# Kernel tuning notes

Hardware: AMD Instinct MI355X
Metric: run time of the kernel (lower is better)

Reference implementation:

```python
import jax, jax.numpy as jnp
import numpy as np

TOP_K = 8
NUM_EXPERTS = 128
HIDDEN = 2048
TOKENS = 16384
NORM_TOPK_PROB = True


def setup_inputs() -> dict:
    key = jax.random.key(0)
    k1, k2 = jax.random.split(key)
    hidden_states = jax.random.normal(k1, (TOKENS, HIDDEN), dtype=jnp.float32)
    # gate weight [num_experts, hidden] (nn.Linear layout)
    weight = jax.random.normal(k2, (NUM_EXPERTS, HIDDEN), dtype=jnp.float32) * 0.02
    return {"hidden_states": hidden_states, "weight": weight}


def reference(hidden_states, weight):
    x = hidden_states.reshape(-1, HIDDEN)
    # router_logits: [tokens, num_experts]
    router_logits = jnp.einsum("td,ed->te", x, weight)
    router_probs = jax.nn.softmax(router_logits.astype(jnp.float32), axis=-1)
    top_vals, top_idx = jax.lax.top_k(router_probs, TOP_K)
    if NORM_TOPK_PROB:
        top_vals = top_vals / jnp.sum(top_vals, axis=-1, keepdims=True)
    top_vals = top_vals.astype(hidden_states.dtype)
    return router_logits, top_vals, top_idx
```

## Files before the change

### kernel.cpp

```cpp
#include <hip/hip_runtime.h>
#include <float.h>
#include <math.h>

#define TOKENS 16384
#define HIDDEN 2048
#define NEXP 128
#define TOPK 8
#define NCAND 12
#define DELTA 5e-4f

#define BM 32
#define BK 64
#define KITERS (HIDDEN / BK)

typedef float f32x16 __attribute__((ext_vector_type(16)));
typedef short bf16x8 __attribute__((ext_vector_type(8)));

__device__ __forceinline__ unsigned pack_hi(float a, float b) {
    return (__float_as_uint(a) >> 16) | (__float_as_uint(b) & 0xFFFF0000u);
}
__device__ __forceinline__ float resid(float a) {
    return a - __uint_as_float(__float_as_uint(a) & 0xFFFF0000u);
}

__device__ __forceinline__ void load_lds_16B(const void* g, void* l) {
    __builtin_amdgcn_global_load_lds(
        (const __attribute__((address_space(1))) unsigned int*)g,
        (__attribute__((address_space(3))) unsigned int*)l, 16, 0, 0);
}

__global__ __launch_bounds__(256) void presplit_w(const float* __restrict__ W,
                                                  unsigned short* __restrict__ Ws) {
    const int c = blockIdx.x * 256 + threadIdx.x;
    const int lane = c & 63;
    const int q = c >> 6;
    const int hl = q & 1;
    const int nt = (q >> 1) & 3;
    const int k16 = q >> 3;
    const int e = nt * 32 + (lane & 31);
    const int k0 = k16 * 16 + (lane >> 5) * 8;
    const float* wp = W + (size_t)e * HIDDEN + k0;
    float4 a = *(const float4*)wp;
    float4 b = *(const float4*)(wp + 4);
    if (hl) {
        a.x = resid(a.x); a.y = resid(a.y); a.z = resid(a.z); a.w = resid(a.w);
        b.x = resid(b.x); b.y = resid(b.y); b.z = resid(b.z); b.w = resid(b.w);
    }
    uint4 o;
    o.x = pack_hi(a.x, a.y); o.y = pack_hi(a.z, a.w);
    o.z = pack_hi(b.x, b.y); o.w = pack_hi(b.z, b.w);
    *(uint4*)(Ws + (size_t)c * 8) = o;
}

__global__ __launch_bounds__(256) void router_gemm(const float* __restrict__ X,
                                                   const unsigned short* __restrict__ Ws,
                                                   float* __restrict__ logits) {
    __shared__ unsigned short sA[8 * 512];
    __shared__ unsigned short sB[32 * 512];
    const int tid = threadIdx.x;
    const int lane = tid & 63;
    const int wid = tid >> 6;
    const int t0 = blockIdx.x * BM;

    const int arow = tid >> 3, aq = tid & 7;
    const int offH = ((aq >> 1) * 2 + 0) * 512 + ((aq & 1) * 32 + arow) * 8;
    const int offL = offH + 512;
    const float* Xp = X + (size_t)(t0 + arow) * HIDDEN + aq * 8;

    f32x16 acc;
#pragma unroll
    for (int r = 0; r < 16; ++r) acc[r] = 0.f;

    float4 xa = *(const float4*)(Xp);
    float4 xb = *(const float4*)(Xp + 4);

#pragma unroll 1
    for (int kt = 0; kt < KITERS; ++kt) {
        __syncthreads();
        {
            const unsigned short* src = Ws + ((size_t)kt * 32 + wid * 8) * 512 + lane * 8;
            unsigned short* dst = &sB[(wid * 8) * 512];
#pragma unroll
            for (int i = 0; i < 8; ++i)
                load_lds_16B(src + i * 512, dst + i * 512);
        }
        {
            uint4 v;
            v.x = pack_hi(xa.x, xa.y); v.y = pack_hi(xa.z, xa.w);
            v.z = pack_hi(xb.x, xb.y); v.w = pack_hi(xb.z, xb.w);
            *(uint4*)&sA[offH] = v;
            v.x = pack_hi(resid(xa.x), resid(xa.y));
            v.y = pack_hi(resid(xa.z), resid(xa.w));
            v.z = pack_hi(resid(xb.x), resid(xb.y));
            v.w = pack_hi(resid(xb.z), resid(xb.w));
            *(uint4*)&sA[offL] = v;
        }
        __syncthreads();

        if (kt + 1 < KITERS) {
            const float* xp = Xp + (kt + 1) * BK;
            xa = *(const float4*)(xp);
            xb = *(const float4*)(xp + 4);
        }

#pragma unroll
        for (int s = 0; s < 4; ++s) {
            const bf16x8 ah = *(const bf16x8*)&sA[(s * 2 + 0) * 512 + lane * 8];
            const bf16x8 al = *(const bf16x8*)&sA[(s * 2 + 1) * 512 + lane * 8];
            const int bb = (s * 8 + wid * 2) * 512 + lane * 8;
            const bf16x8 bh = *(const bf16x8*)&sB[bb];
            const bf16x8 bl = *(const bf16x8*)&sB[bb + 512];
            acc = __builtin_amdgcn_mfma_f32_32x32x16_bf16(ah, bh, acc, 0, 0, 0);
            acc = __builtin_amdgcn_mfma_f32_32x32x16_bf16(ah, bl, acc, 0, 0, 0);
            acc = __builtin_amdgcn_mfma_f32_32x32x16_bf16(al, bh, acc, 0, 0, 0);
        }
    }

    const int e = wid * 32 + (lane & 31);
    const int rbase = 4 * (lane >> 5);
#pragma unroll
    for (int reg = 0; reg < 16; ++reg) {
        const int row = (reg & 3) + 8 * (reg >> 2) + rbase;
        logits[(size_t)(t0 + row) * NEXP + e] = acc[reg];
    }
}

__global__ __launch_bounds__(256) void router_topk(const float* __restrict__ logits,
                                                   const float* __restrict__ X,
                                                   const float* __restrict__ W,
                                                   float* __restrict__ top_vals,
                                                   float* __restrict__ top_idx) {
    const int lane = threadIdx.x & 63;
    const int t = blockIdx.x * 4 + (threadIdx.x >> 6);
    const float* lrow = logits + (size_t)t * NEXP;
    const float l0 = lrow[lane];
    const float l1 = lrow[lane + 64];
    bool r0 = false, r1 = false;
    float vals[NCAND]; int idxs[NCAND];

#pragma unroll
    for (int it = 0; it < TOPK + 1; ++it) {
        const float c0 = r0 ? -FLT_MAX : l0;
        const float c1 = r1 ? -FLT_MAX : l1;
        float v; int id;
        if (c1 > c0) { v = c1; id = lane + 64; }
        else         { v = c0; id = lane; }
#pragma unroll
        for (int off = 1; off < 64; off <<= 1) {
            const float ov = __shfl_xor(v, off);
            const int   oi = __shfl_xor(id, off);
            if (ov > v || (ov == v && oi < id)) { v = ov; id = oi; }
        }
        vals[it] = v; idxs[it] = id;
        if (id == lane) r0 = true;
        else if (id == lane + 64) r1 = true;
    }

    float ming = FLT_MAX;
#pragma unroll
    for (int i = 0; i < TOPK; ++i) ming = fminf(ming, vals[i] - vals[i + 1]);

    if (ming >= DELTA) {
        if (lane == 0) {
            const float m = vals[0];
            float ex[TOPK], s = 0.f;
#pragma unroll
            for (int i = 0; i < TOPK; ++i) { ex[i] = expf(vals[i] - m); s += ex[i]; }
            const float inv = 1.f / s;
#pragma unroll
            for (int i = 0; i < TOPK; ++i) {
                top_vals[(size_t)t * TOPK + i] = ex[i] * inv;
                top_idx[(size_t)t * TOPK + i] = (float)idxs[i];
            }
        }
        return;
    }

#pragma unroll
    for (int it = TOPK + 1; it < NCAND; ++it) {
        const float c0 = r0 ? -FLT_MAX : l0;
        const float c1 = r1 ? -FLT_MAX : l1;
        float v; int id;
        if (c1 > c0) { v = c1; id = lane + 64; }
        else         { v = c0; id = lane; }
#pragma unroll
        for (int off = 1; off < 64; off <<= 1) {
            const float ov = __shfl_xor(v, off);
            const int   oi = __shfl_xor(id, off);
            if (ov > v || (ov == v && oi < id)) { v = ov; id = oi; }
        }
        vals[it] = v; idxs[it] = id;
        if (id == lane) r0 = true;
        else if (id == lane + 64) r1 = true;
    }

    const float* xr = X + (size_t)t * HIDDEN;
    double xd[32];
#pragma unroll
    for (int j = 0; j < 8; ++j) {
        const float4 v = *(const float4*)(xr + j * 256 + lane * 4);
        xd[j * 4 + 0] = (double)v.x; xd[j * 4 + 1] = (double)v.y;
        xd[j * 4 + 2] = (double)v.z; xd[j * 4 + 3] = (double)v.w;
    }
    double acc[NCAND];
#pragma unroll
    for (int c = 0; c < NCAND; ++c) {
        const float* wr = W + (size_t)idxs[c] * HIDDEN;
        double a0 = 0.0, a1 = 0.0;
#pragma unroll
        for (int j = 0; j < 8; ++j) {
            const float4 w = *(const float4*)(wr + j * 256 + lane * 4);
            a0 = fma((double)w.x, xd[j * 4 + 0], a0);
            a1 = fma((double)w.y, xd[j * 4 + 1], a1);
            a0 = fma((double)w.z, xd[j * 4 + 2], a0);
            a1 = fma((double)w.w, xd[j * 4 + 3], a1);
        }
        acc[c] = a0 + a1;
    }
#pragma unroll
    for (int c = 0; c < NCAND; ++c)
#pragma unroll
        for (int off = 1; off < 64; off <<= 1)
            acc[c] += __shfl_xor(acc[c], off);

    int rank[NCAND];
#pragma unroll
    for (int c = 0; c < NCAND; ++c) {
        int r = 0;
#pragma unroll
        for (int m = 0; m < NCAND; ++m)
            if (acc[m] > acc[c] || (acc[m] == acc[c] && idxs[m] < idxs[c])) ++r;
        rank[c] = r;
    }
    double vmax = acc[0];
#pragma unroll
    for (int c = 0; c < NCAND; ++c) if (rank[c] == 0) vmax = acc[c];
    float ex[NCAND], s = 0.f;
#pragma unroll
    for (int c = 0; c < NCAND; ++c) {
        ex[c] = (rank[c] < TOPK) ? expf((float)(acc[c] - vmax)) : 0.f;
        s += ex[c];
    }
    const float inv = 1.f / s;
    if (lane == 0) {
#pragma unroll
        for (int c = 0; c < NCAND; ++c)
            if (rank[c] < TOPK) {
                top_vals[(size_t)t * TOPK + rank[c]] = ex[c] * inv;
                top_idx[(size_t)t * TOPK + rank[c]] = (float)idxs[c];
            }
    }
}

extern "C" void kernel_launch(void* const* d_in, const int* in_sizes, int n_in,
                              void* d_out, int out_size, void* d_ws, size_t ws_size,
                              hipStream_t stream) {
    const float* X = (const float*)d_in[0];
    const float* W = (const float*)d_in[1];
    float* logits = (float*)d_out;
    float* tvals  = logits + (size_t)TOKENS * NEXP;
    float* tidx   = tvals + (size_t)TOKENS * TOPK;

    unsigned short* Wsplit = (unsigned short*)d_ws;

    presplit_w<<<256, 256, 0, stream>>>(W, Wsplit);
    router_gemm<<<TOKENS / BM, 256, 0, stream>>>(X, Wsplit, logits);
    router_topk<<<TOKENS / 4, 256, 0, stream>>>(logits, X, W, tvals, tidx);
}
```

Baseline: 294.9 us.

## Drop LDS staging in router GEMM, load operands directly into registers

The router GEMM no longer stages X and the pre-split W through shared memory. Each wave now loads its own A rows and B fragments straight from global memory into registers, with a 4-deep software prefetch ring and a bare s_barrier per group to keep waves roughly in step. This removes the LDS writes and reads and the two __syncthreads per K tile. In exchange, each of the four waves reloads the same X rows redundantly, which raises global/L2 traffic and register pressure.

```diff
diff --git a/kernel.cpp b/kernel.cpp
--- a/kernel.cpp
+++ b/kernel.cpp
@@ -10,8 +10,7 @@
 #define DELTA 5e-4f
 
 #define BM 32
-#define BK 64
-#define KITERS (HIDDEN / BK)
+#define KSTEPS (HIDDEN / 16)
 
 typedef float f32x16 __attribute__((ext_vector_type(16)));
 typedef short bf16x8 __attribute__((ext_vector_type(8)));
@@ -23,10 +22,17 @@
     return a - __uint_as_float(__float_as_uint(a) & 0xFFFF0000u);
 }
 
-__device__ __forceinline__ void load_lds_16B(const void* g, void* l) {
-    __builtin_amdgcn_global_load_lds(
-        (const __attribute__((address_space(1))) unsigned int*)g,
-        (__attribute__((address_space(3))) unsigned int*)l, 16, 0, 0);
+__device__ __forceinline__ bf16x8 pack8_hi(const float4 a, const float4 b) {
+    union { uint4 u; bf16x8 v; } t;
+    t.u.x = pack_hi(a.x, a.y); t.u.y = pack_hi(a.z, a.w);
+    t.u.z = pack_hi(b.x, b.y); t.u.w = pack_hi(b.z, b.w);
+    return t.v;
+}
+__device__ __forceinline__ bf16x8 pack8_lo(const float4 a, const float4 b) {
+    union { uint4 u; bf16x8 v; } t;
+    t.u.x = pack_hi(resid(a.x), resid(a.y)); t.u.y = pack_hi(resid(a.z), resid(a.w));
+    t.u.z = pack_hi(resid(b.x), resid(b.y)); t.u.w = pack_hi(resid(b.z), resid(b.w));
+    return t.v;
 }
 
 __global__ __launch_bounds__(256) void presplit_w(const float* __restrict__ W,
@@ -55,65 +61,44 @@
 __global__ __launch_bounds__(256) void router_gemm(const float* __restrict__ X,
                                                    const unsigned short* __restrict__ Ws,
                                                    float* __restrict__ logits) {
-    __shared__ unsigned short sA[8 * 512];
-    __shared__ unsigned short sB[32 * 512];
     const int tid = threadIdx.x;
     const int lane = tid & 63;
     const int wid = tid >> 6;
     const int t0 = blockIdx.x * BM;
 
-    const int arow = tid >> 3, aq = tid & 7;
-    const int offH = ((aq >> 1) * 2 + 0) * 512 + ((aq & 1) * 32 + arow) * 8;
-    const int offL = offH + 512;
-    const float* Xp = X + (size_t)(t0 + arow) * HIDDEN + aq * 8;
+    const float* xp = X + (size_t)(t0 + (lane & 31)) * HIDDEN + (lane >> 5) * 8;
+    const unsigned short* bp = Ws + (size_t)(wid * 2) * 512 + (size_t)lane * 8;
 
     f32x16 acc;
 #pragma unroll
     for (int r = 0; r < 16; ++r) acc[r] = 0.f;
 
-    float4 xa = *(const float4*)(Xp);
-    float4 xb = *(const float4*)(Xp + 4);
+    float4 xa[4], xb[4];
+    bf16x8 bh[4], bl[4];
+#pragma unroll
+    for (int i = 0; i < 4; ++i) {
+        xa[i] = *(const float4*)(xp + i * 16);
+        xb[i] = *(const float4*)(xp + i * 16 + 4);
+        bh[i] = *(const bf16x8*)(bp + (size_t)i * 4096);
+        bl[i] = *(const bf16x8*)(bp + (size_t)i * 4096 + 512);
+    }
 
 #pragma unroll 1
-    for (int kt = 0; kt < KITERS; ++kt) {
-        __syncthreads();
-        {
-            const unsigned short* src = Ws + ((size_t)kt * 32 + wid * 8) * 512 + lane * 8;
-            unsigned short* dst = &sB[(wid * 8) * 512];
-#pragma unroll
-            for (int i = 0; i < 8; ++i)
-                load_lds_16B(src + i * 512, dst + i * 512);
-        }
-        {
-            uint4 v;
-            v.x = pack_hi(xa.x, xa.y); v.y = pack_hi(xa.z, xa.w);
-            v.z = pack_hi(xb.x, xb.y); v.w = pack_hi(xb.z, xb.w);
-            *(uint4*)&sA[offH] = v;
-            v.x = pack_hi(resid(xa.x), resid(xa.y));
-            v.y = pack_hi(resid(xa.z), resid(xa.w));
-            v.z = pack_hi(resid(xb.x), resid(xb.y));
-            v.w = pack_hi(resid(xb.z), resid(xb.w));
-            *(uint4*)&sA[offL] = v;
-        }
-        __syncthreads();
-
-        if (kt + 1 < KITERS) {
-            const float* xp = Xp + (kt + 1) * BK;
-            xa = *(const float4*)(xp);
-            xb = *(const float4*)(xp + 4);
-        }
-
-#pragma unroll
-        for (int s = 0; s < 4; ++s) {
-            const bf16x8 ah = *(const bf16x8*)&sA[(s * 2 + 0) * 512 + lane * 8];
-            const bf16x8 al = *(const bf16x8*)&sA[(s * 2 + 1) * 512 + lane * 8];
-            const int bb = (s * 8 + wid * 2) * 512 + lane * 8;
-            const bf16x8 bh = *(const bf16x8*)&sB[bb];
-            const bf16x8 bl = *(const bf16x8*)&sB[bb + 512];
-            acc = __builtin_amdgcn_mfma_f32_32x32x16_bf16(ah, bh, acc, 0, 0, 0);
-            acc = __builtin_amdgcn_mfma_f32_32x32x16_bf16(ah, bl, acc, 0, 0, 0);
-            acc = __builtin_amdgcn_mfma_f32_32x32x16_bf16(al, bh, acc, 0, 0, 0);
-        }
+    for (int kt = 0; kt < KSTEPS; kt += 4) {
+#pragma unroll
+        for (int i = 0; i < 4; ++i) {
+            const bf16x8 ah = pack8_hi(xa[i], xb[i]);
+            const bf16x8 al = pack8_lo(xa[i], xb[i]);
+            acc = __builtin_amdgcn_mfma_f32_32x32x16_bf16(ah, bh[i], acc, 0, 0, 0);
+            acc = __builtin_amdgcn_mfma_f32_32x32x16_bf16(ah, bl[i], acc, 0, 0, 0);
+            acc = __builtin_amdgcn_mfma_f32_32x32x16_bf16(al, bh[i], acc, 0, 0, 0);
+            int kn = kt + 4 + i; if (kn > KSTEPS - 1) kn = KSTEPS - 1;
+            xa[i] = *(const float4*)(xp + kn * 16);
+            xb[i] = *(const float4*)(xp + kn * 16 + 4);
+            bh[i] = *(const bf16x8*)(bp + (size_t)kn * 4096);
+            bl[i] = *(const bf16x8*)(bp + (size_t)kn * 4096 + 512);
+        }
+        __builtin_amdgcn_s_barrier();
     }
 
     const int e = wid * 32 + (lane & 31);
```

Measured after the change: 308.3 us. 1.05x slower.
